# Performance work log

Hardware: AMD Instinct MI355X
Metric: run time of the kernel (lower is better)

Reference implementation:

```python
import jax, jax.numpy as jnp
import numpy as np

K = 3  # knnLoss default k


def _knn_loss(source_pc, target_pc, k=K):
    """Faithful translation of knnLoss.forward.

    For each batch: drop exact-zero (0,0,0) points from both clouds
    (emulated via masking for static shapes), find the k nearest *target*
    points for every *source* point (query=source, ref=target), take the
    mean Euclidean distance, then average over batch.
    """

    def per_batch(src, tgt):  # src, tgt: [N, 3]
        src_valid = jnp.any(src != 0.0, axis=-1)  # [Ns] move_zero_point mask
        tgt_valid = jnp.any(tgt != 0.0, axis=-1)  # [Nt]
        s2 = jnp.sum(src * src, axis=-1)          # [Ns]
        t2 = jnp.sum(tgt * tgt, axis=-1)          # [Nt]
        # squared pairwise distances, [Ns, Nt]
        d2 = s2[:, None] + t2[None, :] - 2.0 * (src @ tgt.T)
        d2 = jnp.maximum(d2, 0.0)
        # invalid (zero) target points can never be a neighbor
        d2 = jnp.where(tgt_valid[None, :], d2, jnp.inf)
        neg_top, _ = jax.lax.top_k(-d2, k)        # k smallest squared dists
        dist = jnp.sqrt(-neg_top)                 # [Ns, k] euclidean, like KNN_CUDA
        # mean over valid source points x k neighbors
        num = jnp.sum(jnp.where(src_valid[:, None], dist, 0.0))
        den = jnp.sum(src_valid).astype(dist.dtype) * k
        return num / den

    return jnp.mean(jax.vmap(per_batch)(source_pc, target_pc))


def setup_inputs() -> dict:
    key = jax.random.key(0)
    k1, k2 = jax.random.split(key)
    B, N = 4, 8192
    source_pc = jax.random.normal(k1, (B, N, 3), dtype=jnp.float32)
    target_pc = jax.random.normal(k2, (B, N, 3), dtype=jnp.float32)
    return {"source_pc": source_pc, "target_pc": target_pc}


def reference(source_pc, target_pc):
    return _knn_loss(source_pc, target_pc)
```

## Files before the change

### kernel.cpp

```cpp
#include <hip/hip_runtime.h>
#include <math.h>

#define BATCH 4
#define NPTS 8192
#define TILE 512
#define NWAVES 16
#define SRC_PER_BLOCK 128
#define NBLOCKS (BATCH * NPTS / SRC_PER_BLOCK)
#define NOCT 64
#define OCTF 32
#define SLOTF (NOCT * OCTF)

typedef __attribute__((ext_vector_type(2))) float f2;

__device__ __forceinline__ float min3f(float a, float b, float c) {
    float d;
    asm("v_min3_f32 %0, %1, %2, %3" : "=v"(d) : "v"(a), "v"(b), "v"(c));
    return d;
}

__device__ __forceinline__ void insert3(float d, float& a0, float& a1, float& a2) {
    float h = fmaxf(a1, d);
    float m = __builtin_amdgcn_fmed3f(a0, a1, d);
    a2 = fminf(a2, h);
    a1 = m;
    a0 = fminf(a0, d);
}

__device__ __forceinline__ void merge33(float a0, float a1, float a2,
                                        float& b0, float& b1, float& b2) {
    float s0 = fminf(a0, b0);
    float h  = fmaxf(a0, b0);
    float m  = fminf(a1, b1);
    float mm = fminf(a2, b2);
    b1 = fminf(h, m);
    b2 = __builtin_amdgcn_fmed3f(h, m, mm);
    b0 = s0;
}

__device__ __forceinline__ void octet_insert(const float4* ob, f2 nx, f2 ny, f2 nz,
                                             float& c0, float& c1, float& c2) {
    float4 X0 = ob[0], X1 = ob[1], Y0 = ob[2], Y1 = ob[3];
    float4 Z0 = ob[4], Z1 = ob[5], W0 = ob[6], W1 = ob[7];
    f2 pa = __builtin_elementwise_fma((f2){Z0.x, Z0.y}, nz, (f2){W0.x, W0.y});
    pa = __builtin_elementwise_fma((f2){Y0.x, Y0.y}, ny, pa);
    pa = __builtin_elementwise_fma((f2){X0.x, X0.y}, nx, pa);
    f2 pb = __builtin_elementwise_fma((f2){Z0.z, Z0.w}, nz, (f2){W0.z, W0.w});
    pb = __builtin_elementwise_fma((f2){Y0.z, Y0.w}, ny, pb);
    pb = __builtin_elementwise_fma((f2){X0.z, X0.w}, nx, pb);
    f2 pc = __builtin_elementwise_fma((f2){Z1.x, Z1.y}, nz, (f2){W1.x, W1.y});
    pc = __builtin_elementwise_fma((f2){Y1.x, Y1.y}, ny, pc);
    pc = __builtin_elementwise_fma((f2){X1.x, X1.y}, nx, pc);
    f2 pd = __builtin_elementwise_fma((f2){Z1.z, Z1.w}, nz, (f2){W1.z, W1.w});
    pd = __builtin_elementwise_fma((f2){Y1.z, Y1.w}, ny, pd);
    pd = __builtin_elementwise_fma((f2){X1.z, X1.w}, nx, pd);
    insert3(pa.x, c0, c1, c2);
    insert3(pa.y, c0, c1, c2);
    insert3(pb.x, c0, c1, c2);
    insert3(pb.y, c0, c1, c2);
    insert3(pc.x, c0, c1, c2);
    insert3(pc.y, c0, c1, c2);
    insert3(pd.x, c0, c1, c2);
    insert3(pd.y, c0, c1, c2);
}

__global__ __launch_bounds__(1024, 4) void knn_fused(const float* __restrict__ src,
                                                     const float* __restrict__ tgt,
                                                     float* __restrict__ acc,
                                                     float* __restrict__ cnt,
                                                     unsigned* __restrict__ ticket,
                                                     float* __restrict__ out) {
    __shared__ float tsf[NWAVES * SLOTF];
    const int tid = threadIdx.x;
    const int lane = tid & 63, wave = tid >> 6;
    const int bid = blockIdx.x;
    const int b = bid >> 6;

    f2 nx[2], ny[2], nz[2];
    #pragma unroll
    for (int s = 0; s < 2; ++s) {
        const float* sp = src + ((size_t)bid * SRC_PER_BLOCK + 64 * s + lane) * 3;
        float ax = sp[0], ay = sp[1], az = sp[2];
        nx[s] = (f2){-2.f * ax, -2.f * ax};
        ny[s] = (f2){-2.f * ay, -2.f * ay};
        nz[s] = (f2){-2.f * az, -2.f * az};
    }

    {
        const float* tb = tgt + ((size_t)b * NPTS + wave * TILE) * 3;
        #pragma unroll
        for (int j = 0; j < 4; ++j) {
            int p = j * 64 + lane;
            const float2* t2 = (const float2*)(tb + 6 * p);
            float2 A = t2[0], Bv = t2[1], C = t2[2];
            float x0 = A.x, y0 = A.y, z0 = Bv.x;
            float x1 = Bv.y, y1 = C.x, z1 = C.y;
            float w0 = x0 * x0 + y0 * y0 + z0 * z0;
            float w1 = x1 * x1 + y1 * y1 + z1 * z1;
            if (!(x0 != 0.f || y0 != 0.f || z0 != 0.f)) w0 = 3.0e38f;
            if (!(x1 != 0.f || y1 != 0.f || z1 != 0.f)) w1 = 3.0e38f;
            int o = p >> 2, k = (2 * p) & 7;
            float* bp = tsf + wave * SLOTF + o * OCTF + k;
            *(float2*)(bp)      = make_float2(x0, x1);
            *(float2*)(bp + 8)  = make_float2(y0, y1);
            *(float2*)(bp + 16) = make_float2(z0, z1);
            *(float2*)(bp + 24) = make_float2(w0, w1);
        }
    }

    float q0[2], q1[2], q2c[2];
    #pragma unroll
    for (int s = 0; s < 2; ++s) { q0[s] = q1[s] = q2c[s] = 3e38f; }

    const float4* tsv = (const float4*)(tsf + wave * SLOTF);
    #pragma unroll 2
    for (int j = 0; j < NOCT; ++j) {
        float4 X0 = tsv[8 * j + 0], X1 = tsv[8 * j + 1];
        float4 Y0 = tsv[8 * j + 2], Y1 = tsv[8 * j + 3];
        float4 Z0 = tsv[8 * j + 4], Z1 = tsv[8 * j + 5];
        float4 W0 = tsv[8 * j + 6], W1 = tsv[8 * j + 7];
        #pragma unroll
        for (int s = 0; s < 2; ++s) {
            f2 pa = __builtin_elementwise_fma((f2){Z0.x, Z0.y}, nz[s], (f2){W0.x, W0.y});
            pa = __builtin_elementwise_fma((f2){Y0.x, Y0.y}, ny[s], pa);
            pa = __builtin_elementwise_fma((f2){X0.x, X0.y}, nx[s], pa);
            f2 pb = __builtin_elementwise_fma((f2){Z0.z, Z0.w}, nz[s], (f2){W0.z, W0.w});
            pb = __builtin_elementwise_fma((f2){Y0.z, Y0.w}, ny[s], pb);
            pb = __builtin_elementwise_fma((f2){X0.z, X0.w}, nx[s], pb);
            f2 pc = __builtin_elementwise_fma((f2){Z1.x, Z1.y}, nz[s], (f2){W1.x, W1.y});
            pc = __builtin_elementwise_fma((f2){Y1.x, Y1.y}, ny[s], pc);
            pc = __builtin_elementwise_fma((f2){X1.x, X1.y}, nx[s], pc);
            f2 pd = __builtin_elementwise_fma((f2){Z1.z, Z1.w}, nz[s], (f2){W1.z, W1.w});
            pd = __builtin_elementwise_fma((f2){Y1.z, Y1.w}, ny[s], pd);
            pd = __builtin_elementwise_fma((f2){X1.z, X1.w}, nx[s], pd);
            float m1 = min3f(pa.x, pa.y, pb.x);
            float m2 = min3f(pb.y, pc.x, pc.y);
            float m3 = min3f(pd.x, pd.y, m1);
            float m4 = fminf(m2, m3);
            unsigned u = (__float_as_uint(m4) & 0xFFFFFFC0u) | (unsigned)j;
            insert3(__uint_as_float(u), q0[s], q1[s], q2c[s]);
        }
    }

    float e0[2], e1[2], e2[2];
    #pragma unroll
    for (int s = 0; s < 2; ++s) {
        e0[s] = 3e38f; e1[s] = 3e38f; e2[s] = 3e38f;
        octet_insert(tsv + 8 * (int)(__float_as_uint(q0[s]) & 63u),
                     nx[s], ny[s], nz[s], e0[s], e1[s], e2[s]);
        octet_insert(tsv + 8 * (int)(__float_as_uint(q1[s]) & 63u),
                     nx[s], ny[s], nz[s], e0[s], e1[s], e2[s]);
        octet_insert(tsv + 8 * (int)(__float_as_uint(q2c[s]) & 63u),
                     nx[s], ny[s], nz[s], e0[s], e1[s], e2[s]);
    }

    __syncthreads();
    #pragma unroll
    for (int s = 0; s < 2; ++s) {
        int base = ((wave * 2 + s) * 64 + lane) * 3;
        tsf[base]     = e0[s];
        tsf[base + 1] = e1[s];
        tsf[base + 2] = e2[s];
    }
    __syncthreads();

    if (tid < 128) {
        int l = tid & 63, srow = tid >> 6;
        int base0 = ((0 * 2 + srow) * 64 + l) * 3;
        float a0 = tsf[base0], a1 = tsf[base0 + 1], a2 = tsf[base0 + 2];
        #pragma unroll
        for (int w = 1; w < NWAVES; ++w) {
            int bse = ((w * 2 + srow) * 64 + l) * 3;
            merge33(tsf[bse], tsf[bse + 1], tsf[bse + 2], a0, a1, a2);
        }
        const float* sp = src + ((size_t)bid * SRC_PER_BLOCK + tid) * 3;
        float sx = sp[0], sy = sp[1], sz = sp[2];
        bool valid = (sx != 0.f) || (sy != 0.f) || (sz != 0.f);
        float qq = sx * sx + sy * sy + sz * sz;
        float sv = valid ? (sqrtf(fmaxf(a0 + qq, 0.f)) + sqrtf(fmaxf(a1 + qq, 0.f)) +
                            sqrtf(fmaxf(a2 + qq, 0.f)))
                         : 0.f;
        float cv = valid ? 1.f : 0.f;
        for (int off = 32; off >= 1; off >>= 1) {
            sv += __shfl_down(sv, off);
            cv += __shfl_down(cv, off);
        }
        if (l == 0) {
            atomicAdd(&acc[b], sv);
            atomicAdd(&cnt[b], cv);
            __threadfence();
        }
    }
    __syncthreads();

    if (tid == 0) {
        unsigned t = atomicAdd(ticket, 1u);
        if (t == (unsigned)(NBLOCKS - 1)) {
            float loss = 0.f;
            #pragma unroll
            for (int bb = 0; bb < BATCH; ++bb) {
                float as = atomicAdd(&acc[bb], 0.f);
                float ac = atomicAdd(&cnt[bb], 0.f);
                loss += as / (ac * 3.0f);
            }
            out[0] = loss * (1.0f / BATCH);
        }
    }
}

extern "C" void kernel_launch(void* const* d_in, const int* in_sizes, int n_in,
                              void* d_out, int out_size, void* d_ws, size_t ws_size,
                              hipStream_t stream) {
    const float* src = (const float*)d_in[0];
    const float* tgt = (const float*)d_in[1];
    float* out = (float*)d_out;

    float* acc = (float*)d_ws;
    float* cnt = acc + 4;
    unsigned* ticket = (unsigned*)((char*)d_ws + 32);

    hipMemsetAsync(d_ws, 0, 64, stream);
    knn_fused<<<dim3(NBLOCKS), 1024, 0, stream>>>(src, tgt, acc, cnt, ticket, out);
}
```

Before: 113.2 us.

## Split targets across block pairs, raise sources per thread, recompute norms

Each thread now handles four source points instead of two, so every target octet read from shared memory is reused across more queries. Each pair of blocks splits a batch's targets in half, and the two halves' top-3 results are merged through global partials with a per-pair ticket. Target squared norms are recomputed in registers instead of stored, which shrinks the shared-memory slot from 8 to 6 (padded 7) float4s per octet. Zero targets are pushed far away via 1e12 coordinates rather than a huge norm. The cost is extra FMAs, an inter-block handshake through global memory, and fewer waves per block (512 threads instead of 1024).

```diff
diff --git a/kernel.cpp b/kernel.cpp
--- a/kernel.cpp
+++ b/kernel.cpp
@@ -4,12 +4,13 @@
 #define BATCH 4
 #define NPTS 8192
 #define TILE 512
-#define NWAVES 16
-#define SRC_PER_BLOCK 128
-#define NBLOCKS (BATCH * NPTS / SRC_PER_BLOCK)
+#define WAVES 8
+#define SPB 256
+#define NBLOCKS 256
 #define NOCT 64
-#define OCTF 32
-#define SLOTF (NOCT * OCTF)
+#define OCT4 7
+#define SLOT4 (NOCT * OCT4)
+#define NPAIRS 128
 
 typedef __attribute__((ext_vector_type(2))) float f2;
 
@@ -38,22 +39,35 @@
     b0 = s0;
 }
 
-__device__ __forceinline__ void octet_insert(const float4* ob, f2 nx, f2 ny, f2 nz,
-                                             float& c0, float& c1, float& c2) {
-    float4 X0 = ob[0], X1 = ob[1], Y0 = ob[2], Y1 = ob[3];
-    float4 Z0 = ob[4], Z1 = ob[5], W0 = ob[6], W1 = ob[7];
-    f2 pa = __builtin_elementwise_fma((f2){Z0.x, Z0.y}, nz, (f2){W0.x, W0.y});
-    pa = __builtin_elementwise_fma((f2){Y0.x, Y0.y}, ny, pa);
-    pa = __builtin_elementwise_fma((f2){X0.x, X0.y}, nx, pa);
-    f2 pb = __builtin_elementwise_fma((f2){Z0.z, Z0.w}, nz, (f2){W0.z, W0.w});
-    pb = __builtin_elementwise_fma((f2){Y0.z, Y0.w}, ny, pb);
-    pb = __builtin_elementwise_fma((f2){X0.z, X0.w}, nx, pb);
-    f2 pc = __builtin_elementwise_fma((f2){Z1.x, Z1.y}, nz, (f2){W1.x, W1.y});
-    pc = __builtin_elementwise_fma((f2){Y1.x, Y1.y}, ny, pc);
-    pc = __builtin_elementwise_fma((f2){X1.x, X1.y}, nx, pc);
-    f2 pd = __builtin_elementwise_fma((f2){Z1.z, Z1.w}, nz, (f2){W1.z, W1.w});
-    pd = __builtin_elementwise_fma((f2){Y1.z, Y1.w}, ny, pd);
-    pd = __builtin_elementwise_fma((f2){X1.z, X1.w}, nx, pd);
+__device__ __forceinline__ void octet_fix(const float4* ob, f2 nx, f2 ny, f2 nz,
+                                          float& c0, float& c1, float& c2) {
+    float4 X0 = ob[0], X1 = ob[1], Y0 = ob[2], Y1 = ob[3], Z0 = ob[4], Z1 = ob[5];
+    f2 xs0 = (f2){X0.x, X0.y}, xs1 = (f2){X0.z, X0.w};
+    f2 xs2 = (f2){X1.x, X1.y}, xs3 = (f2){X1.z, X1.w};
+    f2 ys0 = (f2){Y0.x, Y0.y}, ys1 = (f2){Y0.z, Y0.w};
+    f2 ys2 = (f2){Y1.x, Y1.y}, ys3 = (f2){Y1.z, Y1.w};
+    f2 zs0 = (f2){Z0.x, Z0.y}, zs1 = (f2){Z0.z, Z0.w};
+    f2 zs2 = (f2){Z1.x, Z1.y}, zs3 = (f2){Z1.z, Z1.w};
+    f2 w0 = zs0 * zs0; w0 = __builtin_elementwise_fma(ys0, ys0, w0);
+    w0 = __builtin_elementwise_fma(xs0, xs0, w0);
+    f2 w1 = zs1 * zs1; w1 = __builtin_elementwise_fma(ys1, ys1, w1);
+    w1 = __builtin_elementwise_fma(xs1, xs1, w1);
+    f2 w2 = zs2 * zs2; w2 = __builtin_elementwise_fma(ys2, ys2, w2);
+    w2 = __builtin_elementwise_fma(xs2, xs2, w2);
+    f2 w3 = zs3 * zs3; w3 = __builtin_elementwise_fma(ys3, ys3, w3);
+    w3 = __builtin_elementwise_fma(xs3, xs3, w3);
+    f2 pa = __builtin_elementwise_fma(zs0, nz, w0);
+    pa = __builtin_elementwise_fma(ys0, ny, pa);
+    pa = __builtin_elementwise_fma(xs0, nx, pa);
+    f2 pb = __builtin_elementwise_fma(zs1, nz, w1);
+    pb = __builtin_elementwise_fma(ys1, ny, pb);
+    pb = __builtin_elementwise_fma(xs1, nx, pb);
+    f2 pc = __builtin_elementwise_fma(zs2, nz, w2);
+    pc = __builtin_elementwise_fma(ys2, ny, pc);
+    pc = __builtin_elementwise_fma(xs2, nx, pc);
+    f2 pd = __builtin_elementwise_fma(zs3, nz, w3);
+    pd = __builtin_elementwise_fma(ys3, ny, pd);
+    pd = __builtin_elementwise_fma(xs3, nx, pd);
     insert3(pa.x, c0, c1, c2);
     insert3(pa.y, c0, c1, c2);
     insert3(pb.x, c0, c1, c2);
@@ -64,146 +78,194 @@
     insert3(pd.y, c0, c1, c2);
 }
 
-__global__ __launch_bounds__(1024, 4) void knn_fused(const float* __restrict__ src,
-                                                     const float* __restrict__ tgt,
-                                                     float* __restrict__ acc,
-                                                     float* __restrict__ cnt,
-                                                     unsigned* __restrict__ ticket,
-                                                     float* __restrict__ out) {
-    __shared__ float tsf[NWAVES * SLOTF];
+__global__ __launch_bounds__(512) void knn_fused(const float* __restrict__ src,
+                                                 const float* __restrict__ tgt,
+                                                 float* __restrict__ acc,
+                                                 float* __restrict__ cnt,
+                                                 unsigned* __restrict__ done,
+                                                 unsigned* __restrict__ pairT,
+                                                 float* __restrict__ part,
+                                                 float* __restrict__ out) {
+    __shared__ float tsf[WAVES * SLOT4 * 4];
     const int tid = threadIdx.x;
     const int lane = tid & 63, wave = tid >> 6;
     const int bid = blockIdx.x;
+    const int g = bid >> 1;
+    const int h = bid & 1;
     const int b = bid >> 6;
 
-    f2 nx[2], ny[2], nz[2];
-    #pragma unroll
-    for (int s = 0; s < 2; ++s) {
-        const float* sp = src + ((size_t)bid * SRC_PER_BLOCK + 64 * s + lane) * 3;
+    {
+        const int tI = h * 8 + wave;
+        const float4* tf4 = (const float4*)(tgt +
+            ((size_t)b * NPTS + tI * TILE + lane * 8) * 3);
+        float4 f0 = tf4[0], f1 = tf4[1], f2v = tf4[2];
+        float4 f3 = tf4[3], f4v = tf4[4], f5 = tf4[5];
+        float tx[8], ty[8], tz[8];
+        tx[0] = f0.x;  ty[0] = f0.y;  tz[0] = f0.z;
+        tx[1] = f0.w;  ty[1] = f1.x;  tz[1] = f1.y;
+        tx[2] = f1.z;  ty[2] = f1.w;  tz[2] = f2v.x;
+        tx[3] = f2v.y; ty[3] = f2v.z; tz[3] = f2v.w;
+        tx[4] = f3.x;  ty[4] = f3.y;  tz[4] = f3.z;
+        tx[5] = f3.w;  ty[5] = f4v.x; tz[5] = f4v.y;
+        tx[6] = f4v.z; ty[6] = f4v.w; tz[6] = f5.x;
+        tx[7] = f5.y;  ty[7] = f5.z;  tz[7] = f5.w;
+        #pragma unroll
+        for (int j = 0; j < 8; ++j) {
+            if (!(tx[j] != 0.f || ty[j] != 0.f || tz[j] != 0.f)) {
+                tx[j] = 1e12f; ty[j] = 1e12f; tz[j] = 1e12f;
+            }
+        }
+        float4* slot = ((float4*)tsf) + wave * SLOT4 + lane * OCT4;
+        slot[0] = make_float4(tx[0], tx[1], tx[2], tx[3]);
+        slot[1] = make_float4(tx[4], tx[5], tx[6], tx[7]);
+        slot[2] = make_float4(ty[0], ty[1], ty[2], ty[3]);
+        slot[3] = make_float4(ty[4], ty[5], ty[6], ty[7]);
+        slot[4] = make_float4(tz[0], tz[1], tz[2], tz[3]);
+        slot[5] = make_float4(tz[4], tz[5], tz[6], tz[7]);
+    }
+
+    f2 nx[4], ny[4], nz[4];
+    #pragma unroll
+    for (int s = 0; s < 4; ++s) {
+        const float* sp = src + ((size_t)g * SPB + s * 64 + lane) * 3;
         float ax = sp[0], ay = sp[1], az = sp[2];
         nx[s] = (f2){-2.f * ax, -2.f * ax};
         ny[s] = (f2){-2.f * ay, -2.f * ay};
         nz[s] = (f2){-2.f * az, -2.f * az};
     }
 
-    {
-        const float* tb = tgt + ((size_t)b * NPTS + wave * TILE) * 3;
+    float q0[4], q1[4], q2c[4];
+    #pragma unroll
+    for (int s = 0; s < 4; ++s) { q0[s] = q1[s] = q2c[s] = 3e38f; }
+
+    const float4* tsv = ((const float4*)tsf) + wave * SLOT4;
+    #pragma unroll 2
+    for (int o = 0; o < NOCT; ++o) {
+        float4 X0 = tsv[7 * o + 0], X1 = tsv[7 * o + 1];
+        float4 Y0 = tsv[7 * o + 2], Y1 = tsv[7 * o + 3];
+        float4 Z0 = tsv[7 * o + 4], Z1 = tsv[7 * o + 5];
+        f2 xs0 = (f2){X0.x, X0.y}, xs1 = (f2){X0.z, X0.w};
+        f2 xs2 = (f2){X1.x, X1.y}, xs3 = (f2){X1.z, X1.w};
+        f2 ys0 = (f2){Y0.x, Y0.y}, ys1 = (f2){Y0.z, Y0.w};
+        f2 ys2 = (f2){Y1.x, Y1.y}, ys3 = (f2){Y1.z, Y1.w};
+        f2 zs0 = (f2){Z0.x, Z0.y}, zs1 = (f2){Z0.z, Z0.w};
+        f2 zs2 = (f2){Z1.x, Z1.y}, zs3 = (f2){Z1.z, Z1.w};
+        f2 w0 = zs0 * zs0; w0 = __builtin_elementwise_fma(ys0, ys0, w0);
+        w0 = __builtin_elementwise_fma(xs0, xs0, w0);
+        f2 w1 = zs1 * zs1; w1 = __builtin_elementwise_fma(ys1, ys1, w1);
+        w1 = __builtin_elementwise_fma(xs1, xs1, w1);
+        f2 w2 = zs2 * zs2; w2 = __builtin_elementwise_fma(ys2, ys2, w2);
+        w2 = __builtin_elementwise_fma(xs2, xs2, w2);
+        f2 w3 = zs3 * zs3; w3 = __builtin_elementwise_fma(ys3, ys3, w3);
+        w3 = __builtin_elementwise_fma(xs3, xs3, w3);
         #pragma unroll
-        for (int j = 0; j < 4; ++j) {
-            int p = j * 64 + lane;
-            const float2* t2 = (const float2*)(tb + 6 * p);
-            float2 A = t2[0], Bv = t2[1], C = t2[2];
-            float x0 = A.x, y0 = A.y, z0 = Bv.x;
-            float x1 = Bv.y, y1 = C.x, z1 = C.y;
-            float w0 = x0 * x0 + y0 * y0 + z0 * z0;
-            float w1 = x1 * x1 + y1 * y1 + z1 * z1;
-            if (!(x0 != 0.f || y0 != 0.f || z0 != 0.f)) w0 = 3.0e38f;
-            if (!(x1 != 0.f || y1 != 0.f || z1 != 0.f)) w1 = 3.0e38f;
-            int o = p >> 2, k = (2 * p) & 7;
-            float* bp = tsf + wave * SLOTF + o * OCTF + k;
-            *(float2*)(bp)      = make_float2(x0, x1);
-            *(float2*)(bp + 8)  = make_float2(y0, y1);
-            *(float2*)(bp + 16) = make_float2(z0, z1);
-            *(float2*)(bp + 24) = make_float2(w0, w1);
-        }
-    }
-
-    float q0[2], q1[2], q2c[2];
-    #pragma unroll
-    for (int s = 0; s < 2; ++s) { q0[s] = q1[s] = q2c[s] = 3e38f; }
-
-    const float4* tsv = (const float4*)(tsf + wave * SLOTF);
-    #pragma unroll 2
-    for (int j = 0; j < NOCT; ++j) {
-        float4 X0 = tsv[8 * j + 0], X1 = tsv[8 * j + 1];
-        float4 Y0 = tsv[8 * j + 2], Y1 = tsv[8 * j + 3];
-        float4 Z0 = tsv[8 * j + 4], Z1 = tsv[8 * j + 5];
-        float4 W0 = tsv[8 * j + 6], W1 = tsv[8 * j + 7];
-        #pragma unroll
-        for (int s = 0; s < 2; ++s) {
-            f2 pa = __builtin_elementwise_fma((f2){Z0.x, Z0.y}, nz[s], (f2){W0.x, W0.y});
-            pa = __builtin_elementwise_fma((f2){Y0.x, Y0.y}, ny[s], pa);
-            pa = __builtin_elementwise_fma((f2){X0.x, X0.y}, nx[s], pa);
-            f2 pb = __builtin_elementwise_fma((f2){Z0.z, Z0.w}, nz[s], (f2){W0.z, W0.w});
-            pb = __builtin_elementwise_fma((f2){Y0.z, Y0.w}, ny[s], pb);
-            pb = __builtin_elementwise_fma((f2){X0.z, X0.w}, nx[s], pb);
-            f2 pc = __builtin_elementwise_fma((f2){Z1.x, Z1.y}, nz[s], (f2){W1.x, W1.y});
-            pc = __builtin_elementwise_fma((f2){Y1.x, Y1.y}, ny[s], pc);
-            pc = __builtin_elementwise_fma((f2){X1.x, X1.y}, nx[s], pc);
-            f2 pd = __builtin_elementwise_fma((f2){Z1.z, Z1.w}, nz[s], (f2){W1.z, W1.w});
-            pd = __builtin_elementwise_fma((f2){Y1.z, Y1.w}, ny[s], pd);
-            pd = __builtin_elementwise_fma((f2){X1.z, X1.w}, nx[s], pd);
+        for (int s = 0; s < 4; ++s) {
+            f2 pa = __builtin_elementwise_fma(zs0, nz[s], w0);
+            pa = __builtin_elementwise_fma(ys0, ny[s], pa);
+            pa = __builtin_elementwise_fma(xs0, nx[s], pa);
+            f2 pb = __builtin_elementwise_fma(zs1, nz[s], w1);
+            pb = __builtin_elementwise_fma(ys1, ny[s], pb);
+            pb = __builtin_elementwise_fma(xs1, nx[s], pb);
+            f2 pc = __builtin_elementwise_fma(zs2, nz[s], w2);
+            pc = __builtin_elementwise_fma(ys2, ny[s], pc);
+            pc = __builtin_elementwise_fma(xs2, nx[s], pc);
+            f2 pd = __builtin_elementwise_fma(zs3, nz[s], w3);
+            pd = __builtin_elementwise_fma(ys3, ny[s], pd);
+            pd = __builtin_elementwise_fma(xs3, nx[s], pd);
             float m1 = min3f(pa.x, pa.y, pb.x);
             float m2 = min3f(pb.y, pc.x, pc.y);
             float m3 = min3f(pd.x, pd.y, m1);
             float m4 = fminf(m2, m3);
-            unsigned u = (__float_as_uint(m4) & 0xFFFFFFC0u) | (unsigned)j;
+            unsigned u = (__float_as_uint(m4) & 0xFFFFFFC0u) | (unsigned)o;
             insert3(__uint_as_float(u), q0[s], q1[s], q2c[s]);
         }
     }
 
-    float e0[2], e1[2], e2[2];
-    #pragma unroll
-    for (int s = 0; s < 2; ++s) {
+    float e0[4], e1[4], e2[4];
+    #pragma unroll
+    for (int s = 0; s < 4; ++s) {
         e0[s] = 3e38f; e1[s] = 3e38f; e2[s] = 3e38f;
-        octet_insert(tsv + 8 * (int)(__float_as_uint(q0[s]) & 63u),
-                     nx[s], ny[s], nz[s], e0[s], e1[s], e2[s]);
-        octet_insert(tsv + 8 * (int)(__float_as_uint(q1[s]) & 63u),
-                     nx[s], ny[s], nz[s], e0[s], e1[s], e2[s]);
-        octet_insert(tsv + 8 * (int)(__float_as_uint(q2c[s]) & 63u),
-                     nx[s], ny[s], nz[s], e0[s], e1[s], e2[s]);
-    }
-
-    __syncthreads();
-    #pragma unroll
-    for (int s = 0; s < 2; ++s) {
-        int base = ((wave * 2 + s) * 64 + lane) * 3;
-        tsf[base]     = e0[s];
-        tsf[base + 1] = e1[s];
-        tsf[base + 2] = e2[s];
-    }
-    __syncthreads();
-
-    if (tid < 128) {
-        int l = tid & 63, srow = tid >> 6;
-        int base0 = ((0 * 2 + srow) * 64 + l) * 3;
-        float a0 = tsf[base0], a1 = tsf[base0 + 1], a2 = tsf[base0 + 2];
+        octet_fix(tsv + 7 * (int)(__float_as_uint(q0[s]) & 63u),
+                  nx[s], ny[s], nz[s], e0[s], e1[s], e2[s]);
+        octet_fix(tsv + 7 * (int)(__float_as_uint(q1[s]) & 63u),
+                  nx[s], ny[s], nz[s], e0[s], e1[s], e2[s]);
+        octet_fix(tsv + 7 * (int)(__float_as_uint(q2c[s]) & 63u),
+                  nx[s], ny[s], nz[s], e0[s], e1[s], e2[s]);
+    }
+
+    __syncthreads();
+    #pragma unroll
+    for (int s = 0; s < 4; ++s) {
+        int idx = ((s * 8 + wave) * 64 + lane) * 3;
+        tsf[idx] = e0[s]; tsf[idx + 1] = e1[s]; tsf[idx + 2] = e2[s];
+    }
+    __syncthreads();
+
+    float a0 = 3e38f, a1 = 3e38f, a2 = 3e38f;
+    if (tid < 256) {
+        int s = tid >> 6, l = tid & 63;
+        int base = ((s * 8 + 0) * 64 + l) * 3;
+        a0 = tsf[base]; a1 = tsf[base + 1]; a2 = tsf[base + 2];
         #pragma unroll
-        for (int w = 1; w < NWAVES; ++w) {
-            int bse = ((w * 2 + srow) * 64 + l) * 3;
+        for (int w = 1; w < 8; ++w) {
+            int bse = ((s * 8 + w) * 64 + l) * 3;
             merge33(tsf[bse], tsf[bse + 1], tsf[bse + 2], a0, a1, a2);
         }
-        const float* sp = src + ((size_t)bid * SRC_PER_BLOCK + tid) * 3;
-        float sx = sp[0], sy = sp[1], sz = sp[2];
-        bool valid = (sx != 0.f) || (sy != 0.f) || (sz != 0.f);
-        float qq = sx * sx + sy * sy + sz * sz;
-        float sv = valid ? (sqrtf(fmaxf(a0 + qq, 0.f)) + sqrtf(fmaxf(a1 + qq, 0.f)) +
-                            sqrtf(fmaxf(a2 + qq, 0.f)))
-                         : 0.f;
-        float cv = valid ? 1.f : 0.f;
+        size_t pidx = ((size_t)bid * SPB + tid) * 3;
+        atomicExch(&part[pidx + 0], a0);
+        atomicExch(&part[pidx + 1], a1);
+        atomicExch(&part[pidx + 2], a2);
+    }
+    __threadfence();
+    __syncthreads();
+
+    unsigned* tflag = (unsigned*)(tsf + 8192);
+    if (tid == 0) tflag[0] = atomicAdd(&pairT[g], 1u);
+    __syncthreads();
+    unsigned t = tflag[0];
+
+    if (t == 1u) {
+        float sv = 0.f, cv = 0.f;
+        if (tid < 256) {
+            size_t qidx = ((size_t)(bid ^ 1) * SPB + tid) * 3;
+            float p0 = atomicAdd(&part[qidx + 0], 0.f);
+            float p1 = atomicAdd(&part[qidx + 1], 0.f);
+            float p2 = atomicAdd(&part[qidx + 2], 0.f);
+            merge33(p0, p1, p2, a0, a1, a2);
+            const float* sp = src + ((size_t)g * SPB + tid) * 3;
+            float sx = sp[0], sy = sp[1], sz = sp[2];
+            bool valid = (sx != 0.f) || (sy != 0.f) || (sz != 0.f);
+            float qq = sx * sx + sy * sy + sz * sz;
+            sv = valid ? (sqrtf(fmaxf(a0 + qq, 0.f)) + sqrtf(fmaxf(a1 + qq, 0.f)) +
+                          sqrtf(fmaxf(a2 + qq, 0.f)))
+                       : 0.f;
+            cv = valid ? 1.f : 0.f;
+        }
         for (int off = 32; off >= 1; off >>= 1) {
             sv += __shfl_down(sv, off);
             cv += __shfl_down(cv, off);
         }
-        if (l == 0) {
-            atomicAdd(&acc[b], sv);
-            atomicAdd(&cnt[b], cv);
+        float* red = tsf + 8200;
+        if (lane == 0) { red[wave] = sv; red[wave + 8] = cv; }
+        __syncthreads();
+        if (tid == 0) {
+            float ss = 0.f, cc = 0.f;
+            #pragma unroll
+            for (int w = 0; w < 8; ++w) { ss += red[w]; cc += red[w + 8]; }
+            atomicAdd(&acc[b], ss);
+            atomicAdd(&cnt[b], cc);
             __threadfence();
-        }
-    }
-    __syncthreads();
-
-    if (tid == 0) {
-        unsigned t = atomicAdd(ticket, 1u);
-        if (t == (unsigned)(NBLOCKS - 1)) {
-            float loss = 0.f;
-            #pragma unroll
-            for (int bb = 0; bb < BATCH; ++bb) {
-                float as = atomicAdd(&acc[bb], 0.f);
-                float ac = atomicAdd(&cnt[bb], 0.f);
-                loss += as / (ac * 3.0f);
+            unsigned dt = atomicAdd(done, 1u);
+            if (dt == (unsigned)(NPAIRS - 1)) {
+                float loss = 0.f;
+                #pragma unroll
+                for (int bb = 0; bb < BATCH; ++bb) {
+                    float as = atomicAdd(&acc[bb], 0.f);
+                    float ac = atomicAdd(&cnt[bb], 0.f);
+                    loss += as / (ac * 3.0f);
+                }
+                out[0] = loss * (1.0f / BATCH);
             }
-            out[0] = loss * (1.0f / BATCH);
         }
     }
 }
@@ -217,8 +279,11 @@
 
     float* acc = (float*)d_ws;
     float* cnt = acc + 4;
-    unsigned* ticket = (unsigned*)((char*)d_ws + 32);
-
-    hipMemsetAsync(d_ws, 0, 64, stream);
-    knn_fused<<<dim3(NBLOCKS), 1024, 0, stream>>>(src, tgt, acc, cnt, ticket, out);
-}
+    unsigned* done = (unsigned*)((char*)d_ws + 32);
+    unsigned* pairT = (unsigned*)((char*)d_ws + 64);
+    float* part = (float*)((char*)d_ws + 1024);
+
+    hipMemsetAsync(d_ws, 0, 1024, stream);
+    knn_fused<<<dim3(NBLOCKS), 512, 0, stream>>>(src, tgt, acc, cnt, done,
+                                                 pairT, part, out);
+}
```

Measured after the change: 124.0 us. 1.1x slower.
